# Optimization experiments

Hardware: AMD Instinct MI355X
Metric: run time of the kernel (lower is better)

## Reference

```python
import jax, jax.numpy as jnp
import numpy as np

B, C, N, H = 4, 256, 1024, 8
D = C            # per-head q/k dim (out_channels defaults to in_channels)
DV = C           # per-head value/output dim (y_out_channels defaults to out_channels)


def setup_inputs() -> dict:
    key = jax.random.key(0)
    ks = jax.random.split(key, 10)
    s = 0.02
    return {
        "x": jax.random.normal(ks[0], (B, C, N), jnp.float32),
        "y": jax.random.normal(ks[1], (B, C, N), jnp.float32),
        "Wq": jax.random.normal(ks[2], (H * D, C), jnp.float32) * s,
        "bq": jnp.zeros((H * D,), jnp.float32),
        "Wk": jax.random.normal(ks[3], (H * D, C), jnp.float32) * s,
        "bk": jnp.zeros((H * D,), jnp.float32),
        "Wv": jax.random.normal(ks[4], (H * DV, C), jnp.float32) * s,
        "bv": jnp.zeros((H * DV,), jnp.float32),
        "Wp": jax.random.normal(ks[5], (DV, C), jnp.float32) * s,  # projection, bias=False
        "gamma": jax.random.uniform(ks[6], (H, 1, 1, 1), jnp.float32) + 0.001,
    }


def _pconv(t, W, b):
    # 1x1 conv1d: (O,C) x (B,C,N) -> (B,O,N)
    out = jnp.einsum('oc,bcn->bon', W, t)
    return out if b is None else out + b[None, :, None]


def reference(x, y, Wq, bq, Wk, bk, Wv, bv, Wp, gamma):
    b_, _, n_ = x.shape
    h = gamma.shape[0]
    # Q/K/V projections, split channels into h heads (head-major chunks of D)
    q = _pconv(x, Wq, bq).reshape(b_, h, -1, n_)   # [B,H,D,N]
    k = _pconv(x, Wk, bk).reshape(b_, h, -1, n_)   # [B,H,D,N]
    v = _pconv(y, Wv, bv).reshape(b_, h, -1, n_)   # [B,H,DV,N]
    # energy[i,j] = sum_d q[d,i]*k[d,j]; softmax over keys j (no sqrt(d) scaling)
    attn = jax.nn.softmax(jnp.einsum('bhdn,bhdm->bhnm', q, k), axis=-1)
    out = jnp.einsum('bhdm,bhnm->bhdn', v, attn)   # [B,H,DV,N]
    # residual branch: y projected to DV channels (1x1 conv, no bias)
    yp = jnp.einsum('oc,bcn->bon', Wp, y)          # [B,DV,N]
    g = gamma.reshape(1, h, 1, 1)
    out = (g * out + yp[:, None, :, :]) / (1.0 + g)
    # concat heads along channel dim (head-major), matching split_cat(out,1,0,2)
    return out.reshape(b_, -1, n_)                 # [B,H*DV,N]
```

## Files before the change

### kernel.cpp

```cpp
#include <hip/hip_runtime.h>

#define Bb 4
#define Cc 256
#define Nn 1024
#define Hh 8
#define Oo 2048

typedef __attribute__((ext_vector_type(8))) short bf16x8;
typedef __attribute__((ext_vector_type(4))) float f32x4;

__device__ __forceinline__ short f2bf(float f) {
  unsigned u = __builtin_bit_cast(unsigned, f);
  unsigned r = u + 0x7FFFu + ((u >> 16) & 1u);
  return (short)(r >> 16);
}
__device__ __forceinline__ f32x4 mfma16(bf16x8 a, bf16x8 b, f32x4 c) {
  return __builtin_amdgcn_mfma_f32_16x16x32_bf16(a, b, c, 0, 0, 0);
}
__device__ __forceinline__ void gl_lds16(const void* g, void* l) {
  __builtin_amdgcn_global_load_lds(
      (const __attribute__((address_space(1))) void*)g,
      (__attribute__((address_space(3))) void*)l, 16, 0, 0);
}

__device__ __forceinline__ void stage_row512(const char* gbase, char* lds,
                                             int wave, int lane) {
#pragma unroll
  for (int i = 0; i < 8; i++) {
    int off = (wave * 8 + i) * 1024;
    int L = off + lane * 16;
    int r = L >> 9;
    int c = ((L >> 4) & 31) ^ (r & 7);
    gl_lds16(gbase + r * 512 + c * 16, lds + off);
  }
}
__device__ __forceinline__ void stage_v(const char* Vg, char* lds, int k0,
                                        int wave, int lane) {
#pragma unroll
  for (int i = 0; i < 8; i++) {
    int off = (wave * 8 + i) * 1024;
    int L = off + lane * 16;
    int r = L >> 7;
    int c = ((L >> 4) & 7) ^ (r & 7);
    gl_lds16(Vg + (size_t)r * 2048 + k0 * 2 + c * 16, lds + off);
  }
}

__global__ __launch_bounds__(256) void k_pack(const float* __restrict__ src,
                                              short* __restrict__ dst, int n) {
  int i = (blockIdx.x * 256 + threadIdx.x) * 4;
  if (i + 3 < n) {
    float4 v = *(const float4*)(src + i);
    short4 o;
    o.x = f2bf(v.x);
    o.y = f2bf(v.y);
    o.z = f2bf(v.z);
    o.w = f2bf(v.w);
    *(short4*)(dst + i) = o;
  }
}

__global__ __launch_bounds__(256) void k_transpose(
    const float* __restrict__ x, const float* __restrict__ y,
    short* __restrict__ xT, short* __restrict__ yT) {
  int bz = blockIdx.z;
  int b = bz >> 1;
  const float* src = (bz & 1) ? y : x;
  short* dst = (bz & 1) ? yT : xT;
  src += (size_t)b * Cc * Nn;
  dst += (size_t)b * Nn * Cc;
  __shared__ short tile[64][72];
  int n0 = blockIdx.x * 64, c0 = blockIdx.y * 64;
  int t = threadIdx.x;
#pragma unroll
  for (int i = 0; i < 16; i++) {
    int idx = t + i * 256;
    int cc = idx >> 6, nn = idx & 63;
    tile[cc][nn] = f2bf(src[(size_t)(c0 + cc) * Nn + n0 + nn]);
  }
  __syncthreads();
#pragma unroll
  for (int i = 0; i < 16; i++) {
    int idx = t + i * 256;
    int nn = idx >> 6, cc = idx & 63;
    dst[(size_t)(n0 + nn) * Cc + c0 + cc] = tile[cc][nn];
  }
}

__global__ __launch_bounds__(256) void k_proj_qk(
    const short* __restrict__ xT, const short* __restrict__ Wq,
    const float* __restrict__ bq, const short* __restrict__ Wk,
    const float* __restrict__ bk, short* __restrict__ Qt,
    short* __restrict__ Kt) {
  int b = blockIdx.z, n0 = blockIdx.x * 64, o0 = blockIdx.y * 64;
  int wave = threadIdx.x >> 6, lane = threadIdx.x & 63;
  int quad = lane >> 4, l16 = lane & 15;
  int sw = l16 & 7;
  __shared__ short Wqs[64 * 256];
  __shared__ short Wks[64 * 256];

  stage_row512((const char*)(Wq + (size_t)o0 * Cc), (char*)Wqs, wave, lane);
  stage_row512((const char*)(Wk + (size_t)o0 * Cc), (char*)Wks, wave, lane);
  const short* aptr =
      xT + (size_t)b * Nn * Cc + (size_t)(n0 + wave * 16 + l16) * Cc + quad * 8;
  bf16x8 areg[8];
#pragma unroll
  for (int ks = 0; ks < 8; ks++) areg[ks] = *(const bf16x8*)(aptr + ks * 32);

  f32x4 accQ[4], accK[4];
#pragma unroll
  for (int j = 0; j < 4; j++) {
    accQ[j] = f32x4{0.f, 0.f, 0.f, 0.f};
    accK[j] = f32x4{0.f, 0.f, 0.f, 0.f};
  }
  __syncthreads();
#pragma unroll
  for (int ks = 0; ks < 8; ks++) {
#pragma unroll
    for (int cj = 0; cj < 4; cj++) {
      int off = (cj * 16 + l16) * 512 + (((ks * 4 + quad) ^ sw) << 4);
      bf16x8 wqf = *(const bf16x8*)((const char*)Wqs + off);
      bf16x8 wkf = *(const bf16x8*)((const char*)Wks + off);
      accQ[cj] = mfma16(areg[ks], wqf, accQ[cj]);
      accK[cj] = mfma16(areg[ks], wkf, accK[cj]);
    }
  }
#pragma unroll
  for (int cj = 0; cj < 4; cj++) {
    int o = o0 + cj * 16 + l16;
    int h = o >> 8, d = o & 255;
    float vbq = bq[o];
    float vbk = bk[o];
#pragma unroll
    for (int r = 0; r < 4; r++) {
      int n = n0 + wave * 16 + quad * 4 + r;
      size_t idx = (((size_t)(b * Hh + h) * Nn) + n) * 256 + d;
      Qt[idx] = f2bf(accQ[cj][r] + vbq);
      Kt[idx] = f2bf(accK[cj][r] + vbk);
    }
  }
}

template <bool FP32OUT>
__global__ __launch_bounds__(256) void k_proj_on(
    const short* __restrict__ yTs, const short* __restrict__ W,
    const float* __restrict__ bias, void* __restrict__ outp, int Ot) {
  int b = blockIdx.z, n0 = blockIdx.x * 64, o0 = blockIdx.y * 64;
  int wave = threadIdx.x >> 6, lane = threadIdx.x & 63;
  int quad = lane >> 4, l16 = lane & 15;
  int sw = l16 & 7;
  __shared__ short Ys[64 * 256];

  stage_row512((const char*)(yTs + (size_t)b * Nn * Cc + (size_t)n0 * Cc),
               (char*)Ys, wave, lane);
  const short* aptr = W + (size_t)(o0 + wave * 16 + l16) * Cc + quad * 8;
  bf16x8 areg[8];
#pragma unroll
  for (int ks = 0; ks < 8; ks++) areg[ks] = *(const bf16x8*)(aptr + ks * 32);

  f32x4 acc[4];
#pragma unroll
  for (int j = 0; j < 4; j++) acc[j] = f32x4{0.f, 0.f, 0.f, 0.f};
  __syncthreads();
#pragma unroll
  for (int ks = 0; ks < 8; ks++) {
#pragma unroll
    for (int cj = 0; cj < 4; cj++) {
      bf16x8 bb = *(const bf16x8*)((const char*)Ys + (cj * 16 + l16) * 512 +
                                   (((ks * 4 + quad) ^ sw) << 4));
      acc[cj] = mfma16(areg[ks], bb, acc[cj]);
    }
  }
#pragma unroll
  for (int cj = 0; cj < 4; cj++) {
    int n = n0 + cj * 16 + l16;
#pragma unroll
    for (int r = 0; r < 4; r++) {
      int o = o0 + wave * 16 + quad * 4 + r;
      float v = acc[cj][r] + (bias ? bias[o] : 0.f);
      size_t idx = ((size_t)b * Ot + o) * Nn + n;
      if (FP32OUT)
        ((float*)outp)[idx] = v;
      else
        ((short*)outp)[idx] = f2bf(v);
    }
  }
}

__global__ __launch_bounds__(256) void k_attn(
    const short* __restrict__ Qt, const short* __restrict__ Kt,
    const short* __restrict__ Vv, const float* __restrict__ yp,
    const float* __restrict__ gamma, float* __restrict__ out) {
  int id = blockIdx.x;
  int bh = (id & 7) * 4 + (id >> 7);
  int q0 = ((id >> 3) & 15) * 64;
  int b = bh >> 3, h = bh & 7;
  int wave = threadIdx.x >> 6, lane = threadIdx.x & 63;
  int quad = lane >> 4, l16 = lane & 15;
  int sw = l16 & 7;
  const short* Qb = Qt + (size_t)bh * Nn * 256;
  const char* Kg = (const char*)(Kt + (size_t)bh * Nn * 256);
  const char* Vg = (const char*)(Vv + (size_t)bh * 256 * Nn);

  __shared__ short Klds[64 * 256];
  __shared__ short Vlds[256 * 64];
  __shared__ short plds[4][16][72];

  bf16x8 qreg[8];
  {
    const short* qp = Qb + (size_t)(q0 + wave * 16 + l16) * 256 + quad * 8;
#pragma unroll
    for (int ks = 0; ks < 8; ks++) qreg[ks] = *(const bf16x8*)(qp + ks * 32);
  }
  f32x4 oacc[16];
#pragma unroll
  for (int j = 0; j < 16; j++) oacc[j] = f32x4{0.f, 0.f, 0.f, 0.f};
  float m_i[4], l_i[4];
#pragma unroll
  for (int r = 0; r < 4; r++) {
    m_i[r] = -1e30f;
    l_i[r] = 0.f;
  }

  stage_row512(Kg, (char*)Klds, wave, lane);
  stage_v(Vg, (char*)Vlds, 0, wave, lane);

  for (int kt = 0; kt < 16; kt++) {
    int k0 = kt * 64;
    __syncthreads();
    f32x4 sc[4];
#pragma unroll
    for (int j = 0; j < 4; j++) sc[j] = f32x4{0.f, 0.f, 0.f, 0.f};
#pragma unroll
    for (int ks = 0; ks < 8; ks++) {
#pragma unroll
      for (int cj = 0; cj < 4; cj++) {
        bf16x8 kb = *(const bf16x8*)((const char*)Klds +
                                     (cj * 16 + l16) * 512 +
                                     (((ks * 4 + quad) ^ sw) << 4));
        sc[cj] = mfma16(qreg[ks], kb, sc[cj]);
      }
    }
    float alpha[4];
#pragma unroll
    for (int r = 0; r < 4; r++) {
      float v = fmaxf(fmaxf(sc[0][r], sc[1][r]), fmaxf(sc[2][r], sc[3][r]));
      v = fmaxf(v, __shfl_xor(v, 1));
      v = fmaxf(v, __shfl_xor(v, 2));
      v = fmaxf(v, __shfl_xor(v, 4));
      v = fmaxf(v, __shfl_xor(v, 8));
      float mn = fmaxf(m_i[r], v);
      alpha[r] = __expf(m_i[r] - mn);
      m_i[r] = mn;
    }
    float rs[4] = {0.f, 0.f, 0.f, 0.f};
#pragma unroll
    for (int cj = 0; cj < 4; cj++) {
#pragma unroll
      for (int r = 0; r < 4; r++) {
        float p = __expf(sc[cj][r] - m_i[r]);
        rs[r] += p;
        plds[wave][quad * 4 + r][cj * 16 + l16] = f2bf(p);
      }
    }
#pragma unroll
    for (int r = 0; r < 4; r++) {
      float v = rs[r];
      v += __shfl_xor(v, 1);
      v += __shfl_xor(v, 2);
      v += __shfl_xor(v, 4);
      v += __shfl_xor(v, 8);
      l_i[r] = l_i[r] * alpha[r] + v;
    }
#pragma unroll
    for (int j = 0; j < 16; j++)
#pragma unroll
      for (int r = 0; r < 4; r++) oacc[j][r] *= alpha[r];
    __syncthreads();
    if (kt < 15) stage_row512(Kg + (size_t)(k0 + 64) * 512, (char*)Klds, wave, lane);
    bf16x8 ap0 = *(const bf16x8*)&plds[wave][l16][quad * 8];
    bf16x8 ap1 = *(const bf16x8*)&plds[wave][l16][32 + quad * 8];
#pragma unroll
    for (int dj = 0; dj < 16; dj++) {
      const char* vrow = (const char*)Vlds + (dj * 16 + l16) * 128;
      bf16x8 v0 = *(const bf16x8*)(vrow + ((quad ^ sw) << 4));
      bf16x8 v1 = *(const bf16x8*)(vrow + (((quad + 4) ^ sw) << 4));
      oacc[dj] = mfma16(ap0, v0, oacc[dj]);
      oacc[dj] = mfma16(ap1, v1, oacc[dj]);
    }
    __syncthreads();
    if (kt < 15) stage_v(Vg, (char*)Vlds, k0 + 64, wave, lane);
  }
  float gf = gamma[h];
  float sg = gf / (1.f + gf), sy = 1.f / (1.f + gf);
  int qq = q0 + wave * 16 + quad * 4;
#pragma unroll
  for (int dj = 0; dj < 16; dj++) {
    int dv = dj * 16 + l16;
    const float* ypp = yp + ((size_t)b * 256 + dv) * Nn + qq;
    float* op = out + ((size_t)b * Oo + h * 256 + dv) * Nn + qq;
    float4 yv = *(const float4*)ypp;
    float4 ov;
    ov.x = sg * (oacc[dj][0] / l_i[0]) + sy * yv.x;
    ov.y = sg * (oacc[dj][1] / l_i[1]) + sy * yv.y;
    ov.z = sg * (oacc[dj][2] / l_i[2]) + sy * yv.z;
    ov.w = sg * (oacc[dj][3] / l_i[3]) + sy * yv.w;
    *(float4*)op = ov;
  }
}

extern "C" void kernel_launch(void* const* d_in, const int* in_sizes, int n_in,
                              void* d_out, int out_size, void* d_ws,
                              size_t ws_size, hipStream_t stream) {
  const float* x = (const float*)d_in[0];
  const float* y = (const float*)d_in[1];
  const float* Wq = (const float*)d_in[2];
  const float* bq = (const float*)d_in[3];
  const float* Wk = (const float*)d_in[4];
  const float* bk = (const float*)d_in[5];
  const float* Wv = (const float*)d_in[6];
  const float* bv = (const float*)d_in[7];
  const float* Wp = (const float*)d_in[8];
  const float* gamma = (const float*)d_in[9];
  float* out = (float*)d_out;

  char* w = (char*)d_ws;
  short* Qt = (short*)(w + 0);
  short* Kt = (short*)(w + 16777216);
  short* Vv = (short*)(w + 33554432);
  short* xT = (short*)(w + 50331648);
  short* yT = (short*)(w + 52428800);
  float* yp = (float*)(w + 54525952);
  short* Wqb = (short*)(w + 58720256);
  short* Wkb = (short*)(w + 59768832);
  short* Wvb = (short*)(w + 60817408);
  short* Wpb = (short*)(w + 61865984);

  k_pack<<<dim3(512), dim3(256), 0, stream>>>(Wq, Wqb, Oo * Cc);
  k_pack<<<dim3(512), dim3(256), 0, stream>>>(Wk, Wkb, Oo * Cc);
  k_pack<<<dim3(512), dim3(256), 0, stream>>>(Wv, Wvb, Oo * Cc);
  k_pack<<<dim3(64), dim3(256), 0, stream>>>(Wp, Wpb, Cc * Cc);
  k_transpose<<<dim3(Nn / 64, Cc / 64, 2 * Bb), dim3(256), 0, stream>>>(
      x, y, xT, yT);
  k_proj_qk<<<dim3(Nn / 64, Oo / 64, Bb), dim3(256), 0, stream>>>(
      xT, Wqb, bq, Wkb, bk, Qt, Kt);
  k_proj_on<false><<<dim3(Nn / 64, Oo / 64, Bb), dim3(256), 0, stream>>>(
      yT, Wvb, bv, (void*)Vv, Oo);
  k_proj_on<true><<<dim3(Nn / 64, Cc / 64, Bb), dim3(256), 0, stream>>>(
      yT, Wpb, nullptr, (void*)yp, Cc);
  k_attn<<<dim3(512), dim3(256), 0, stream>>>(Qt, Kt, Vv, yp, gamma, out);
}
```

Measured before the change: 207.2 us.

## Split PV across waves by DV slice, read V from global, fuse small launches

The attention kernel no longer stages V into LDS. Each wave now owns a 64-wide slice of the value dimension for all 64 queries, reads V fragments straight from global memory, and takes every wave's P tile and rescale factors from shared memory. The aim is to cut LDS staging traffic and one barrier per key tile, at the cost of uncoalesced-ish global V loads and an extra barrier for sharing alpha. It also merges the four weight-pack launches into one and the V and Wp projections into one launch to reduce launch overhead.

Result: slower. 236.8 us (median of 2 runs) (+14.3%).

```diff
diff --git a/kernel.cpp b/kernel.cpp
--- a/kernel.cpp
+++ b/kernel.cpp
@@ -34,30 +34,33 @@
     gl_lds16(gbase + r * 512 + c * 16, lds + off);
   }
 }
-__device__ __forceinline__ void stage_v(const char* Vg, char* lds, int k0,
-                                        int wave, int lane) {
-#pragma unroll
-  for (int i = 0; i < 8; i++) {
-    int off = (wave * 8 + i) * 1024;
-    int L = off + lane * 16;
-    int r = L >> 7;
-    int c = ((L >> 4) & 7) ^ (r & 7);
-    gl_lds16(Vg + (size_t)r * 2048 + k0 * 2 + c * 16, lds + off);
-  }
-}
-
-__global__ __launch_bounds__(256) void k_pack(const float* __restrict__ src,
-                                              short* __restrict__ dst, int n) {
+
+__global__ __launch_bounds__(256) void k_pack4(
+    const float* __restrict__ Wq, const float* __restrict__ Wk,
+    const float* __restrict__ Wv, const float* __restrict__ Wp,
+    short* __restrict__ dWq, short* __restrict__ dWk, short* __restrict__ dWv,
+    short* __restrict__ dWp) {
+  const int NW = Oo * Cc;
   int i = (blockIdx.x * 256 + threadIdx.x) * 4;
-  if (i + 3 < n) {
-    float4 v = *(const float4*)(src + i);
-    short4 o;
-    o.x = f2bf(v.x);
-    o.y = f2bf(v.y);
-    o.z = f2bf(v.z);
-    o.w = f2bf(v.w);
-    *(short4*)(dst + i) = o;
-  }
+  const float* src;
+  short* dst;
+  int off;
+  if (i < NW) {
+    src = Wq; dst = dWq; off = i;
+  } else if (i < 2 * NW) {
+    src = Wk; dst = dWk; off = i - NW;
+  } else if (i < 3 * NW) {
+    src = Wv; dst = dWv; off = i - 2 * NW;
+  } else {
+    src = Wp; dst = dWp; off = i - 3 * NW;
+  }
+  float4 v = *(const float4*)(src + off);
+  short4 o;
+  o.x = f2bf(v.x);
+  o.y = f2bf(v.y);
+  o.z = f2bf(v.z);
+  o.w = f2bf(v.w);
+  *(short4*)(dst + off) = o;
 }
 
 __global__ __launch_bounds__(256) void k_transpose(
@@ -141,11 +144,15 @@
   }
 }
 
-template <bool FP32OUT>
-__global__ __launch_bounds__(256) void k_proj_on(
-    const short* __restrict__ yTs, const short* __restrict__ W,
-    const float* __restrict__ bias, void* __restrict__ outp, int Ot) {
-  int b = blockIdx.z, n0 = blockIdx.x * 64, o0 = blockIdx.y * 64;
+__global__ __launch_bounds__(256) void k_proj_v(
+    const short* __restrict__ yTs, const short* __restrict__ Wv,
+    const float* __restrict__ bv, const short* __restrict__ Wp,
+    short* __restrict__ Vv, float* __restrict__ yp) {
+  int b = blockIdx.z, n0 = blockIdx.x * 64;
+  int by = blockIdx.y;
+  bool isP = by >= 32;
+  const short* W = isP ? Wp : Wv;
+  int o0 = (isP ? (by - 32) : by) * 64;
   int wave = threadIdx.x >> 6, lane = threadIdx.x & 63;
   int quad = lane >> 4, l16 = lane & 15;
   int sw = l16 & 7;
@@ -177,12 +184,12 @@
 #pragma unroll
     for (int r = 0; r < 4; r++) {
       int o = o0 + wave * 16 + quad * 4 + r;
-      float v = acc[cj][r] + (bias ? bias[o] : 0.f);
-      size_t idx = ((size_t)b * Ot + o) * Nn + n;
-      if (FP32OUT)
-        ((float*)outp)[idx] = v;
-      else
-        ((short*)outp)[idx] = f2bf(v);
+      if (isP) {
+        yp[((size_t)b * Cc + o) * Nn + n] = acc[cj][r];
+      } else {
+        float v = acc[cj][r] + bv[o];
+        Vv[((size_t)b * Oo + o) * Nn + n] = f2bf(v);
+      }
     }
   }
 }
@@ -200,11 +207,12 @@
   int sw = l16 & 7;
   const short* Qb = Qt + (size_t)bh * Nn * 256;
   const char* Kg = (const char*)(Kt + (size_t)bh * Nn * 256);
-  const char* Vg = (const char*)(Vv + (size_t)bh * 256 * Nn);
+  const short* Vb = Vv + (size_t)bh * 256 * Nn;
 
   __shared__ short Klds[64 * 256];
-  __shared__ short Vlds[256 * 64];
   __shared__ short plds[4][16][72];
+  __shared__ float alds[64];
+  __shared__ float llds[64];
 
   bf16x8 qreg[8];
   {
@@ -223,7 +231,6 @@
   }
 
   stage_row512(Kg, (char*)Klds, wave, lane);
-  stage_v(Vg, (char*)Vlds, 0, wave, lane);
 
   for (int kt = 0; kt < 16; kt++) {
     int k0 = kt * 64;
@@ -241,7 +248,7 @@
         sc[cj] = mfma16(qreg[ks], kb, sc[cj]);
       }
     }
-    float alpha[4];
+    f32x4 alpha;
 #pragma unroll
     for (int r = 0; r < 4; r++) {
       float v = fmaxf(fmaxf(sc[0][r], sc[1][r]), fmaxf(sc[2][r], sc[3][r]));
@@ -272,40 +279,63 @@
       v += __shfl_xor(v, 8);
       l_i[r] = l_i[r] * alpha[r] + v;
     }
+    if (l16 == 0) *(f32x4*)&alds[wave * 16 + quad * 4] = alpha;
+    __syncthreads();
+    if (kt < 15)
+      stage_row512(Kg + (size_t)(k0 + 64) * 512, (char*)Klds, wave, lane);
+    f32x4 av[4];
+#pragma unroll
+    for (int qb = 0; qb < 4; qb++) av[qb] = *(const f32x4*)&alds[qb * 16 + quad * 4];
 #pragma unroll
     for (int j = 0; j < 16; j++)
 #pragma unroll
-      for (int r = 0; r < 4; r++) oacc[j][r] *= alpha[r];
-    __syncthreads();
-    if (kt < 15) stage_row512(Kg + (size_t)(k0 + 64) * 512, (char*)Klds, wave, lane);
-    bf16x8 ap0 = *(const bf16x8*)&plds[wave][l16][quad * 8];
-    bf16x8 ap1 = *(const bf16x8*)&plds[wave][l16][32 + quad * 8];
-#pragma unroll
-    for (int dj = 0; dj < 16; dj++) {
-      const char* vrow = (const char*)Vlds + (dj * 16 + l16) * 128;
-      bf16x8 v0 = *(const bf16x8*)(vrow + ((quad ^ sw) << 4));
-      bf16x8 v1 = *(const bf16x8*)(vrow + (((quad + 4) ^ sw) << 4));
-      oacc[dj] = mfma16(ap0, v0, oacc[dj]);
-      oacc[dj] = mfma16(ap1, v1, oacc[dj]);
-    }
-    __syncthreads();
-    if (kt < 15) stage_v(Vg, (char*)Vlds, k0 + 64, wave, lane);
-  }
+      for (int r = 0; r < 4; r++) oacc[j][r] *= av[j >> 2][r];
+    bf16x8 ap0[4], ap1[4];
+#pragma unroll
+    for (int qb = 0; qb < 4; qb++) {
+      ap0[qb] = *(const bf16x8*)&plds[qb][l16][quad * 8];
+      ap1[qb] = *(const bf16x8*)&plds[qb][l16][32 + quad * 8];
+    }
+#pragma unroll
+    for (int dj = 0; dj < 4; dj++) {
+      const short* vp =
+          Vb + (size_t)(wave * 64 + dj * 16 + l16) * Nn + k0 + quad * 8;
+      bf16x8 v0 = *(const bf16x8*)vp;
+      bf16x8 v1 = *(const bf16x8*)(vp + 32);
+#pragma unroll
+      for (int qb = 0; qb < 4; qb++) {
+        oacc[qb * 4 + dj] = mfma16(ap0[qb], v0, oacc[qb * 4 + dj]);
+        oacc[qb * 4 + dj] = mfma16(ap1[qb], v1, oacc[qb * 4 + dj]);
+      }
+    }
+  }
+  if (l16 == 0) {
+    f32x4 lv;
+#pragma unroll
+    for (int r = 0; r < 4; r++) lv[r] = l_i[r];
+    *(f32x4*)&llds[wave * 16 + quad * 4] = lv;
+  }
+  __syncthreads();
   float gf = gamma[h];
   float sg = gf / (1.f + gf), sy = 1.f / (1.f + gf);
-  int qq = q0 + wave * 16 + quad * 4;
-#pragma unroll
-  for (int dj = 0; dj < 16; dj++) {
-    int dv = dj * 16 + l16;
-    const float* ypp = yp + ((size_t)b * 256 + dv) * Nn + qq;
-    float* op = out + ((size_t)b * Oo + h * 256 + dv) * Nn + qq;
-    float4 yv = *(const float4*)ypp;
-    float4 ov;
-    ov.x = sg * (oacc[dj][0] / l_i[0]) + sy * yv.x;
-    ov.y = sg * (oacc[dj][1] / l_i[1]) + sy * yv.y;
-    ov.z = sg * (oacc[dj][2] / l_i[2]) + sy * yv.z;
-    ov.w = sg * (oacc[dj][3] / l_i[3]) + sy * yv.w;
-    *(float4*)op = ov;
+#pragma unroll
+  for (int qb = 0; qb < 4; qb++) {
+    f32x4 lv = *(const f32x4*)&llds[qb * 16 + quad * 4];
+    int qq = q0 + qb * 16 + quad * 4;
+#pragma unroll
+    for (int dj = 0; dj < 4; dj++) {
+      int dv = wave * 64 + dj * 16 + l16;
+      const float* ypp = yp + ((size_t)b * 256 + dv) * Nn + qq;
+      float* op = out + ((size_t)b * Oo + h * 256 + dv) * Nn + qq;
+      float4 yv = *(const float4*)ypp;
+      f32x4 oa = oacc[qb * 4 + dj];
+      float4 ov;
+      ov.x = sg * (oa[0] / lv[0]) + sy * yv.x;
+      ov.y = sg * (oa[1] / lv[1]) + sy * yv.y;
+      ov.z = sg * (oa[2] / lv[2]) + sy * yv.z;
+      ov.w = sg * (oa[3] / lv[3]) + sy * yv.w;
+      *(float4*)op = ov;
+    }
   }
 }
 
@@ -336,17 +366,13 @@
   short* Wvb = (short*)(w + 60817408);
   short* Wpb = (short*)(w + 61865984);
 
-  k_pack<<<dim3(512), dim3(256), 0, stream>>>(Wq, Wqb, Oo * Cc);
-  k_pack<<<dim3(512), dim3(256), 0, stream>>>(Wk, Wkb, Oo * Cc);
-  k_pack<<<dim3(512), dim3(256), 0, stream>>>(Wv, Wvb, Oo * Cc);
-  k_pack<<<dim3(64), dim3(256), 0, stream>>>(Wp, Wpb, Cc * Cc);
+  k_pack4<<<dim3(1600), dim3(256), 0, stream>>>(Wq, Wk, Wv, Wp, Wqb, Wkb, Wvb,
+                                                Wpb);
   k_transpose<<<dim3(Nn / 64, Cc / 64, 2 * Bb), dim3(256), 0, stream>>>(
       x, y, xT, yT);
   k_proj_qk<<<dim3(Nn / 64, Oo / 64, Bb), dim3(256), 0, stream>>>(
       xT, Wqb, bq, Wkb, bk, Qt, Kt);
-  k_proj_on<false><<<dim3(Nn / 64, Oo / 64, Bb), dim3(256), 0, stream>>>(
-      yT, Wvb, bv, (void*)Vv, Oo);
-  k_proj_on<true><<<dim3(Nn / 64, Cc / 64, Bb), dim3(256), 0, stream>>>(
-      yT, Wpb, nullptr, (void*)yp, Cc);
+  k_proj_v<<<dim3(Nn / 64, 36, Bb), dim3(256), 0, stream>>>(yT, Wvb, bv, Wpb,
+                                                            Vv, yp);
   k_attn<<<dim3(512), dim3(256), 0, stream>>>(Qt, Kt, Vv, yp, gamma, out);
 }
```
